# Performance work log

Measured on AMD Instinct MI355X. Metric: run time of the kernel, lower is better.

## Reference

```python
import jax, jax.numpy as jnp
import numpy as np


def setup_inputs() -> dict:
    key = jax.random.key(0)
    ks = jax.random.split(key, 7)
    LAG, N, NREG, NT, H = 5, 4096, 500, 500, 16
    s = 0.05  # keep activations in a sane range
    return {
        "AX": jax.random.normal(ks[0], (LAG, N, NREG), dtype=jnp.float32),
        "W0": jax.random.normal(ks[1], (H * NT, NREG, LAG), dtype=jnp.float32) * s,
        "b0": jax.random.normal(ks[2], (H * NT,), dtype=jnp.float32) * s,
        "W1": jax.random.normal(ks[3], (NT, H, H), dtype=jnp.float32) * s,
        "b1": jax.random.normal(ks[4], (NT, H), dtype=jnp.float32) * s,
        "W2": jax.random.normal(ks[5], (NT, 1, H), dtype=jnp.float32) * s,
        "b2": jax.random.normal(ks[6], (NT, 1), dtype=jnp.float32) * s,
    }


def reference(AX, W0, b0, W1, b1, W2, b2):
    # First layer: sum_i AX[i] @ W0[:,:,lag-1-i].T + b0, fused over lag.
    # AX: [lag, N, n_regs]; W0: [hidden0*n_targets, n_regs, lag]
    x = jnp.einsum('lnr,orl->no', AX, W0[:, :, ::-1]) + b0  # [N, hidden0*nt]
    N = x.shape[0]
    nt, d1, d0 = W1.shape  # [n_targets, d_out, d_in]
    # Grouped 1x1 convs == independent per-target GEMMs; channels are target-major.
    x = x.reshape(N, nt, d0)
    x = jax.nn.relu(x)
    x = jnp.einsum('ntd,ted->nte', x, W1) + b1  # [N, nt, d1]
    x = jax.nn.relu(x)
    x = jnp.einsum('nte,tfe->ntf', x, W2) + b2  # [N, nt, 1]
    return x[..., 0]  # [N, n_targets]
```

## Files before the change

kernel.cpp:

```cpp
#include <hip/hip_runtime.h>
#include <hip/hip_bf16.h>
#include <stdint.h>

#define LAG 5
#define NROW 4096
#define NREG 500
#define NTGT 500
#define O_REAL 8000
#define KP 2560
#define NPAD 8192
#define BK 64
#define NT 40

typedef __bf16 bf16x8 __attribute__((ext_vector_type(8)));
typedef float f32x4 __attribute__((ext_vector_type(4)));

__device__ __forceinline__ unsigned short f2bf(float f) {
  unsigned u = __float_as_uint(f);
  return (unsigned short)((u + 0x7fffu + ((u >> 16) & 1u)) >> 16);
}

__device__ __forceinline__ void async16(void* lds_base, const void* g) {
  __builtin_amdgcn_global_load_lds(
      (const __attribute__((address_space(1))) unsigned int*)g,
      (__attribute__((address_space(3))) unsigned int*)lds_base,
      16, 0, 0);
}

__global__ __launch_bounds__(256) void convA(const float* __restrict__ AX,
                                             unsigned short* __restrict__ Ab) {
  int idx = blockIdx.x * 256 + threadIdx.x;
  if (idx >= NROW * (KP / 4)) return;
  int n = idx / (KP / 4);
  int c4 = idx - n * (KP / 4);
  int k = c4 * 4;
  ushort4 o;
  if (k < LAG * NREG) {
    int l = k / NREG, r = k - l * NREG;
    float4 v = *(const float4*)(AX + ((size_t)l * NROW + n) * NREG + r);
    o.x = f2bf(v.x); o.y = f2bf(v.y); o.z = f2bf(v.z); o.w = f2bf(v.w);
  } else {
    o.x = 0; o.y = 0; o.z = 0; o.w = 0;
  }
  *(ushort4*)(Ab + (size_t)idx * 4) = o;
}

__global__ __launch_bounds__(256) void convB(const float* __restrict__ W0,
                                             unsigned short* __restrict__ Bb) {
  int idx = blockIdx.x * 256 + threadIdx.x;
  if (idx >= O_REAL * NREG) return;
  int o = idx / NREG, r = idx - o * NREG;
  const float* s = W0 + (size_t)idx * LAG;
  #pragma unroll
  for (int j = 0; j < LAG; ++j)
    Bb[(size_t)o * KP + (size_t)(LAG - 1 - j) * NREG + r] = f2bf(s[j]);
}

__global__ __launch_bounds__(256) void padB(unsigned short* __restrict__ Bb) {
  int idx = blockIdx.x * 256 + threadIdx.x;
  const int A4 = O_REAL * 15;
  ushort4 z; z.x = 0; z.y = 0; z.z = 0; z.w = 0;
  if (idx < A4) {
    int row = idx / 15, c4 = idx - row * 15;
    *(ushort4*)(Bb + (size_t)row * KP + 2500 + c4 * 4) = z;
  } else {
    int j = idx - A4;
    if (j < 192 * (KP / 4))
      *(ushort4*)(Bb + (size_t)O_REAL * KP + (size_t)j * 4) = z;
  }
}

__global__ __launch_bounds__(512, 2) void gemm8(const unsigned short* __restrict__ A,
                                                const unsigned short* __restrict__ B,
                                                const float* __restrict__ b0,
                                                const float* __restrict__ W1g,
                                                const float* __restrict__ b1g,
                                                const float* __restrict__ W2g,
                                                const float* __restrict__ b2g,
                                                float* __restrict__ out) {
  extern __shared__ char smem[];
  char* sAc = smem;
  char* sBc = smem + 65536;

  int bid = blockIdx.x;
  int swz = (bid & 7) * 64 + (bid >> 3);
  int mt = swz & 15, ntile = swz >> 4;
  int row0 = mt * 256, col0 = ntile * 256;

  int tid = threadIdx.x, l = tid & 63, w = tid >> 6;
  int wr = w >> 2, wc = w & 3;

  int sr = l >> 3;
  int ss = (l & 7) ^ sr;
  const unsigned short* gApre0 = A + (size_t)(row0 + (w * 2 + 0) * 8 + sr) * KP + ss * 8;
  const unsigned short* gApre1 = A + (size_t)(row0 + (w * 2 + 1) * 8 + sr) * KP + ss * 8;
  const unsigned short* gBpre0 = B + (size_t)(col0 + (w * 2 + 0) * 8 + sr) * KP + ss * 8;
  const unsigned short* gBpre1 = B + (size_t)(col0 + (w * 2 + 1) * 8 + sr) * KP + ss * 8;

#define STG_A(buf, half, t) do { \
    async16(sAc + (buf) * 32768 + (half) * 16384 + (w * 2 + 0) * 1024, gApre0 + (size_t)(half) * 128 * KP + (size_t)(t) * BK); \
    async16(sAc + (buf) * 32768 + (half) * 16384 + (w * 2 + 1) * 1024, gApre1 + (size_t)(half) * 128 * KP + (size_t)(t) * BK); \
  } while (0)
#define STG_B(buf, half, t) do { \
    async16(sBc + (buf) * 32768 + (half) * 16384 + (w * 2 + 0) * 1024, gBpre0 + (size_t)(half) * 128 * KP + (size_t)(t) * BK); \
    async16(sBc + (buf) * 32768 + (half) * 16384 + (w * 2 + 1) * 1024, gBpre1 + (size_t)(half) * 128 * KP + (size_t)(t) * BK); \
  } while (0)

  int arowb = (wr * 128 + (l & 15)) * 128;
  int browb = (wc * 64 + (l & 15)) * 128;
  int c0 = (((l >> 4) << 4)) ^ ((l & 7) << 4);

  auto lda = [&](int buf, int mi, int kk) -> bf16x8 {
    return *(const bf16x8*)(sAc + buf * 32768 + arowb + mi * 2048 + (c0 ^ (kk * 64)));
  };
  auto ldb = [&](int buf, int ni, int kk) -> bf16x8 {
    return *(const bf16x8*)(sBc + buf * 32768 + browb + ni * 2048 + (c0 ^ (kk * 64)));
  };

  f32x4 acc[8][4];
  #pragma unroll
  for (int i = 0; i < 8; ++i)
    #pragma unroll
    for (int j = 0; j < 4; ++j) acc[i][j] = (f32x4){0.f, 0.f, 0.f, 0.f};

#define PH_SYNC() do { __builtin_amdgcn_s_barrier(); \
    asm volatile("s_waitcnt lgkmcnt(0)" ::: "memory"); \
    __builtin_amdgcn_s_setprio(1); } while (0)
#define PH_END() do { __builtin_amdgcn_s_setprio(0); __builtin_amdgcn_s_barrier(); } while (0)

#define MFMA_Q(MOFF, AF, NIOFF) do { \
    _Pragma("unroll") \
    for (int mi = 0; mi < 4; ++mi) { \
      _Pragma("unroll") \
      for (int ni = 0; ni < 2; ++ni) { \
        acc[(MOFF) + mi][(NIOFF) + ni] = __builtin_amdgcn_mfma_f32_16x16x32_bf16(AF[mi][0], bb[(NIOFF) + ni][0], acc[(MOFF) + mi][(NIOFF) + ni], 0, 0, 0); \
        acc[(MOFF) + mi][(NIOFF) + ni] = __builtin_amdgcn_mfma_f32_16x16x32_bf16(AF[mi][1], bb[(NIOFF) + ni][1], acc[(MOFF) + mi][(NIOFF) + ni], 0, 0, 0); \
      } \
    } \
  } while (0)

  STG_B(0, 0, 0); STG_B(0, 1, 0); STG_A(0, 0, 0); STG_A(0, 1, 0);
  STG_B(1, 0, 1); STG_B(1, 1, 1); STG_A(1, 0, 1);
  asm volatile("s_waitcnt vmcnt(6)" ::: "memory");
  __builtin_amdgcn_s_barrier();

  for (int t = 0; t < NT; t += 2) {
    const bool last = (t == NT - 2);
    bf16x8 a03[4][2], a47[4][2], bb[4][2];

    #pragma unroll
    for (int ni = 0; ni < 4; ++ni) { bb[ni][0] = ldb(0, ni, 0); bb[ni][1] = ldb(0, ni, 1); }
    #pragma unroll
    for (int mi = 0; mi < 4; ++mi) { a03[mi][0] = lda(0, mi, 0); a03[mi][1] = lda(0, mi, 1); }
    STG_A(1, 1, t + 1);
    PH_SYNC(); MFMA_Q(0, a03, 0); PH_END();

    #pragma unroll
    for (int mi = 0; mi < 4; ++mi) { a47[mi][0] = lda(0, 4 + mi, 0); a47[mi][1] = lda(0, 4 + mi, 1); }
    if (!last) STG_B(0, 0, t + 2);
    PH_SYNC(); MFMA_Q(0, a03, 2); PH_END();

    if (!last) STG_B(0, 1, t + 2);
    PH_SYNC(); MFMA_Q(4, a47, 0); PH_END();

    if (!last) STG_A(0, 0, t + 2);
    if (last) asm volatile("s_waitcnt vmcnt(0)" ::: "memory");
    else      asm volatile("s_waitcnt vmcnt(6)" ::: "memory");
    __builtin_amdgcn_s_barrier();
    asm volatile("s_waitcnt lgkmcnt(0)" ::: "memory");
    __builtin_amdgcn_s_setprio(1);
    MFMA_Q(4, a47, 2);
    PH_END();

    #pragma unroll
    for (int ni = 0; ni < 4; ++ni) { bb[ni][0] = ldb(1, ni, 0); bb[ni][1] = ldb(1, ni, 1); }
    #pragma unroll
    for (int mi = 0; mi < 4; ++mi) { a03[mi][0] = lda(1, mi, 0); a03[mi][1] = lda(1, mi, 1); }
    if (!last) STG_A(0, 1, t + 2);
    PH_SYNC(); MFMA_Q(0, a03, 0); PH_END();

    #pragma unroll
    for (int mi = 0; mi < 4; ++mi) { a47[mi][0] = lda(1, 4 + mi, 0); a47[mi][1] = lda(1, 4 + mi, 1); }
    if (!last) STG_B(1, 0, t + 3);
    PH_SYNC(); MFMA_Q(0, a03, 2); PH_END();

    if (!last) STG_B(1, 1, t + 3);
    PH_SYNC(); MFMA_Q(4, a47, 0); PH_END();

    if (!last) STG_A(1, 0, t + 3);
    if (!last) asm volatile("s_waitcnt vmcnt(6)" ::: "memory");
    __builtin_amdgcn_s_barrier();
    asm volatile("s_waitcnt lgkmcnt(0)" ::: "memory");
    __builtin_amdgcn_s_setprio(1);
    MFMA_Q(4, a47, 2);
    __builtin_amdgcn_s_setprio(0);
    __builtin_amdgcn_s_barrier();
  }

  int lq = l >> 4, lr = l & 15;
  int t0 = col0 >> 4;

  float bias[4];
  #pragma unroll
  for (int ni = 0; ni < 4; ++ni) {
    int gcol = col0 + wc * 64 + ni * 16 + lr;
    bias[ni] = (gcol < O_REAL) ? b0[gcol] : 0.f;
  }

  #pragma unroll
  for (int mi = 0; mi < 8; ++mi) {
    #pragma unroll
    for (int ni = 0; ni < 4; ++ni) {
      #pragma unroll
      for (int r = 0; r < 4; ++r) {
        int rowL = wr * 128 + mi * 16 + lq * 4 + r;
        int colL = wc * 64 + ni * 16 + lr;
        int sw = ((rowL ^ (rowL >> 2)) & 7) << 4;
        float v = fmaxf(acc[mi][ni][r] + bias[ni], 0.f);
        *(unsigned short*)(smem + (size_t)rowL * 512 + ((colL * 2) ^ sw)) = f2bf(v);
      }
    }
  }
  __syncthreads();

  int uw = __builtin_amdgcn_readfirstlane(w);
  float oacc[2][4];
  #pragma unroll
  for (int g = 0; g < 2; ++g) {
    int tloc = uw * 2 + g;
    int tt = t0 + tloc;
    bool tvalid = (tt < NTGT);
    const float* w1t = W1g + (size_t)tt * 256;
    float b1v[16], w2v[16];
    float b2v = 0.f;
    if (tvalid) {
      #pragma unroll
      for (int e4 = 0; e4 < 4; ++e4) {
        float4 ba = *(const float4*)(b1g + (size_t)tt * 16 + e4 * 4);
        float4 wa = *(const float4*)(W2g + (size_t)tt * 16 + e4 * 4);
        b1v[e4 * 4 + 0] = ba.x; b1v[e4 * 4 + 1] = ba.y; b1v[e4 * 4 + 2] = ba.z; b1v[e4 * 4 + 3] = ba.w;
        w2v[e4 * 4 + 0] = wa.x; w2v[e4 * 4 + 1] = wa.y; w2v[e4 * 4 + 2] = wa.z; w2v[e4 * 4 + 3] = wa.w;
      }
      b2v = b2g[tt];
    }
    #pragma unroll
    for (int rg = 0; rg < 4; ++rg) {
      int rowL = rg * 64 + l;
      int sw = ((rowL ^ (rowL >> 2)) & 7) << 4;
      const char* bp = smem + (size_t)rowL * 512;
      uint4 va = *(const uint4*)(bp + ((tloc * 32) ^ sw));
      uint4 vb = *(const uint4*)(bp + ((tloc * 32 + 16) ^ sw));
      unsigned q0 = va.x, q1 = va.y, q2 = va.z, q3 = va.w;
      unsigned q4 = vb.x, q5 = vb.y, q6 = vb.z, q7 = vb.w;
      float x[16];
      x[0]  = __uint_as_float(q0 << 16); x[1]  = __uint_as_float(q0 & 0xffff0000u);
      x[2]  = __uint_as_float(q1 << 16); x[3]  = __uint_as_float(q1 & 0xffff0000u);
      x[4]  = __uint_as_float(q2 << 16); x[5]  = __uint_as_float(q2 & 0xffff0000u);
      x[6]  = __uint_as_float(q3 << 16); x[7]  = __uint_as_float(q3 & 0xffff0000u);
      x[8]  = __uint_as_float(q4 << 16); x[9]  = __uint_as_float(q4 & 0xffff0000u);
      x[10] = __uint_as_float(q5 << 16); x[11] = __uint_as_float(q5 & 0xffff0000u);
      x[12] = __uint_as_float(q6 << 16); x[13] = __uint_as_float(q6 & 0xffff0000u);
      x[14] = __uint_as_float(q7 << 16); x[15] = __uint_as_float(q7 & 0xffff0000u);
      float o = 0.f;
      if (tvalid) {
        #pragma unroll
        for (int e = 0; e < 16; ++e) {
          float4 wq0 = *(const float4*)(w1t + e * 16 + 0);
          float4 wq1 = *(const float4*)(w1t + e * 16 + 4);
          float4 wq2 = *(const float4*)(w1t + e * 16 + 8);
          float4 wq3 = *(const float4*)(w1t + e * 16 + 12);
          float s = b1v[e];
          s = fmaf(x[0],  wq0.x, s); s = fmaf(x[1],  wq0.y, s);
          s = fmaf(x[2],  wq0.z, s); s = fmaf(x[3],  wq0.w, s);
          s = fmaf(x[4],  wq1.x, s); s = fmaf(x[5],  wq1.y, s);
          s = fmaf(x[6],  wq1.z, s); s = fmaf(x[7],  wq1.w, s);
          s = fmaf(x[8],  wq2.x, s); s = fmaf(x[9],  wq2.y, s);
          s = fmaf(x[10], wq2.z, s); s = fmaf(x[11], wq2.w, s);
          s = fmaf(x[12], wq3.x, s); s = fmaf(x[13], wq3.y, s);
          s = fmaf(x[14], wq3.z, s); s = fmaf(x[15], wq3.w, s);
          s = fmaxf(s, 0.f);
          o = fmaf(s, w2v[e], o);
        }
        o += b2v;
      }
      oacc[g][rg] = o;
    }
  }
  __syncthreads();

  {
    float* sOut = (float*)smem;
    #pragma unroll
    for (int g = 0; g < 2; ++g) {
      int tloc = uw * 2 + g;
      #pragma unroll
      for (int rg = 0; rg < 4; ++rg)
        sOut[(rg * 64 + l) * 17 + tloc] = oacc[g][rg];
    }
    __syncthreads();
    int c = tid & 15, rr = tid >> 4;
    bool cv = (t0 + c < NTGT);
    #pragma unroll
    for (int j = 0; j < 8; ++j) {
      int row = rr + 32 * j;
      if (cv) out[(size_t)(row0 + row) * NTGT + (t0 + c)] = sOut[row * 17 + c];
    }
  }
#undef STG_A
#undef STG_B
#undef PH_SYNC
#undef PH_END
#undef MFMA_Q
}

extern "C" void kernel_launch(void* const* d_in, const int* in_sizes, int n_in,
                              void* d_out, int out_size, void* d_ws, size_t ws_size,
                              hipStream_t stream) {
  const float* AX = (const float*)d_in[0];
  const float* W0 = (const float*)d_in[1];
  const float* b0 = (const float*)d_in[2];
  const float* W1 = (const float*)d_in[3];
  const float* b1 = (const float*)d_in[4];
  const float* W2 = (const float*)d_in[5];
  const float* b2 = (const float*)d_in[6];
  float* out = (float*)d_out;

  char* ws = (char*)d_ws;
  const size_t szA = (size_t)NROW * KP * 2;
  unsigned short* Ab = (unsigned short*)ws;
  unsigned short* Bb = (unsigned short*)(ws + szA);

  hipFuncSetAttribute((const void*)gemm8, hipFuncAttributeMaxDynamicSharedMemorySize, 131072);

  convA<<<(NROW * (KP / 4) + 255) / 256, 256, 0, stream>>>(AX, Ab);
  convB<<<(O_REAL * NREG + 255) / 256, 256, 0, stream>>>(W0, Bb);
  {
    int npad4 = O_REAL * 15 + 192 * (KP / 4);
    padB<<<(npad4 + 255) / 256, 256, 0, stream>>>(Bb);
  }
  gemm8<<<(NROW / 256) * (NPAD / 256), 512, 131072, stream>>>(Ab, Bb, b0, W1, b1, W2, b2, out);
}
```

Before: 226.8 us.

## Restructure GEMM main loop to prefetch next-stage LDS fragments across barriers

Reorganizes the double-buffered bf16 MFMA main loop so the first A and B fragments of the next LDS stage are read right after the final MFMA quarter of the current stage, before the closing barrier, instead of at the start of each half-iteration. B fragment reads are split into two halves interleaved between MFMA phases. Global-to-LDS stages are regrouped into pairs, with vmcnt thresholds raised from 6 to 8 to match. The aim is to hide LDS read latency and reduce stalls at phase boundaries, at the cost of keeping more fragment registers live across iterations and changing which loads are outstanding at each wait.

```diff
diff --git a/kernel.cpp b/kernel.cpp
--- a/kernel.cpp
+++ b/kernel.cpp
@@ -140,60 +140,69 @@
   } while (0)
 
   STG_B(0, 0, 0); STG_B(0, 1, 0); STG_A(0, 0, 0); STG_A(0, 1, 0);
-  STG_B(1, 0, 1); STG_B(1, 1, 1); STG_A(1, 0, 1);
-  asm volatile("s_waitcnt vmcnt(6)" ::: "memory");
+  STG_B(1, 0, 1); STG_B(1, 1, 1); STG_A(1, 0, 1); STG_A(1, 1, 1);
+  asm volatile("s_waitcnt vmcnt(8)" ::: "memory");
   __builtin_amdgcn_s_barrier();
+
+  bf16x8 a03[4][2], a47[4][2], bb[4][2];
+  #pragma unroll
+  for (int ni = 0; ni < 2; ++ni) { bb[ni][0] = ldb(0, ni, 0); bb[ni][1] = ldb(0, ni, 1); }
+  #pragma unroll
+  for (int mi = 0; mi < 4; ++mi) { a03[mi][0] = lda(0, mi, 0); a03[mi][1] = lda(0, mi, 1); }
 
   for (int t = 0; t < NT; t += 2) {
     const bool last = (t == NT - 2);
-    bf16x8 a03[4][2], a47[4][2], bb[4][2];
-
-    #pragma unroll
-    for (int ni = 0; ni < 4; ++ni) { bb[ni][0] = ldb(0, ni, 0); bb[ni][1] = ldb(0, ni, 1); }
-    #pragma unroll
-    for (int mi = 0; mi < 4; ++mi) { a03[mi][0] = lda(0, mi, 0); a03[mi][1] = lda(0, mi, 1); }
-    STG_A(1, 1, t + 1);
+
     PH_SYNC(); MFMA_Q(0, a03, 0); PH_END();
 
     #pragma unroll
+    for (int ni = 2; ni < 4; ++ni) { bb[ni][0] = ldb(0, ni, 0); bb[ni][1] = ldb(0, ni, 1); }
+    PH_SYNC(); MFMA_Q(0, a03, 2); PH_END();
+
+    #pragma unroll
     for (int mi = 0; mi < 4; ++mi) { a47[mi][0] = lda(0, 4 + mi, 0); a47[mi][1] = lda(0, 4 + mi, 1); }
-    if (!last) STG_B(0, 0, t + 2);
-    PH_SYNC(); MFMA_Q(0, a03, 2); PH_END();
-
-    if (!last) STG_B(0, 1, t + 2);
+    if (!last) { STG_B(0, 0, t + 2); STG_B(0, 1, t + 2); }
     PH_SYNC(); MFMA_Q(4, a47, 0); PH_END();
 
-    if (!last) STG_A(0, 0, t + 2);
+    if (!last) { STG_A(0, 0, t + 2); STG_A(0, 1, t + 2); }
     if (last) asm volatile("s_waitcnt vmcnt(0)" ::: "memory");
-    else      asm volatile("s_waitcnt vmcnt(6)" ::: "memory");
-    __builtin_amdgcn_s_barrier();
-    asm volatile("s_waitcnt lgkmcnt(0)" ::: "memory");
-    __builtin_amdgcn_s_setprio(1);
-    MFMA_Q(4, a47, 2);
-    PH_END();
-
-    #pragma unroll
-    for (int ni = 0; ni < 4; ++ni) { bb[ni][0] = ldb(1, ni, 0); bb[ni][1] = ldb(1, ni, 1); }
-    #pragma unroll
-    for (int mi = 0; mi < 4; ++mi) { a03[mi][0] = lda(1, mi, 0); a03[mi][1] = lda(1, mi, 1); }
-    if (!last) STG_A(0, 1, t + 2);
-    PH_SYNC(); MFMA_Q(0, a03, 0); PH_END();
-
-    #pragma unroll
-    for (int mi = 0; mi < 4; ++mi) { a47[mi][0] = lda(1, 4 + mi, 0); a47[mi][1] = lda(1, 4 + mi, 1); }
-    if (!last) STG_B(1, 0, t + 3);
-    PH_SYNC(); MFMA_Q(0, a03, 2); PH_END();
-
-    if (!last) STG_B(1, 1, t + 3);
-    PH_SYNC(); MFMA_Q(4, a47, 0); PH_END();
-
-    if (!last) STG_A(1, 0, t + 3);
-    if (!last) asm volatile("s_waitcnt vmcnt(6)" ::: "memory");
+    else      asm volatile("s_waitcnt vmcnt(8)" ::: "memory");
     __builtin_amdgcn_s_barrier();
     asm volatile("s_waitcnt lgkmcnt(0)" ::: "memory");
     __builtin_amdgcn_s_setprio(1);
     MFMA_Q(4, a47, 2);
     __builtin_amdgcn_s_setprio(0);
+    #pragma unroll
+    for (int ni = 0; ni < 2; ++ni) { bb[ni][0] = ldb(1, ni, 0); bb[ni][1] = ldb(1, ni, 1); }
+    #pragma unroll
+    for (int mi = 0; mi < 4; ++mi) { a03[mi][0] = lda(1, mi, 0); a03[mi][1] = lda(1, mi, 1); }
+    __builtin_amdgcn_s_barrier();
+
+    PH_SYNC(); MFMA_Q(0, a03, 0); PH_END();
+
+    #pragma unroll
+    for (int ni = 2; ni < 4; ++ni) { bb[ni][0] = ldb(1, ni, 0); bb[ni][1] = ldb(1, ni, 1); }
+    PH_SYNC(); MFMA_Q(0, a03, 2); PH_END();
+
+    #pragma unroll
+    for (int mi = 0; mi < 4; ++mi) { a47[mi][0] = lda(1, 4 + mi, 0); a47[mi][1] = lda(1, 4 + mi, 1); }
+    if (!last) { STG_B(1, 0, t + 3); STG_B(1, 1, t + 3); }
+    PH_SYNC(); MFMA_Q(4, a47, 0); PH_END();
+
+    if (!last) { STG_A(1, 0, t + 3); STG_A(1, 1, t + 3); }
+    if (last) asm volatile("s_waitcnt vmcnt(0)" ::: "memory");
+    else      asm volatile("s_waitcnt vmcnt(8)" ::: "memory");
+    __builtin_amdgcn_s_barrier();
+    asm volatile("s_waitcnt lgkmcnt(0)" ::: "memory");
+    __builtin_amdgcn_s_setprio(1);
+    MFMA_Q(4, a47, 2);
+    __builtin_amdgcn_s_setprio(0);
+    if (!last) {
+      #pragma unroll
+      for (int ni = 0; ni < 2; ++ni) { bb[ni][0] = ldb(0, ni, 0); bb[ni][1] = ldb(0, ni, 1); }
+      #pragma unroll
+      for (int mi = 0; mi < 4; ++mi) { a03[mi][0] = lda(0, mi, 0); a03[mi][1] = lda(0, mi, 1); }
+    }
     __builtin_amdgcn_s_barrier();
   }
 
```

After: 246.8 us. +8.8%, slower.
